# Kernel optimization log

Measured on AMD Instinct MI355X. Metric: run time of the kernel, lower is better.

The kernel has to match this reference:

```python
import jax, jax.numpy as jnp
import numpy as np
import math

B, S, L = 16, 512, 2400
TEXT_DIM, MAX_LEN, N_LAYERS = 64, 256, 6
LN_EPS = 1e-5


def conv1d(x, w, b, pad):
    # x: (B, Cin, W), w: (Cout, Cin, K) -> (B, Cout, W)
    y = jax.lax.conv_general_dilated(x, w, (1,), [(pad, pad)],
                                     dimension_numbers=('NCH', 'OIH', 'NCH'))
    if b is not None:
        y = y + b[None, :, None]
    return y


def setup_inputs() -> dict:
    key = jax.random.key(0)
    ks = jax.random.split(key, 16)
    inv_l = 1.0 / math.sqrt(L)
    inv_t = 1.0 / math.sqrt(TEXT_DIM)
    return {
        "slices": jax.random.normal(ks[0], (B, S, L), jnp.float32),
        "text_codes": jax.random.uniform(ks[1], (B, MAX_LEN), dtype=jnp.float32),
        # TextCondEncoder params
        "tc1_w": jax.random.normal(ks[2], (64, 1, 7), jnp.float32) * (1.0 / math.sqrt(7)),
        "tc1_b": jnp.zeros((64,), jnp.float32),
        "tc2_w": jax.random.normal(ks[3], (128, 64, 5), jnp.float32) * (1.0 / math.sqrt(64 * 5)),
        "tc2_b": jnp.zeros((128,), jnp.float32),
        "tc3_w": jax.random.normal(ks[4], (TEXT_DIM, 128, 3), jnp.float32) * (1.0 / math.sqrt(128 * 3)),
        "tc3_b": jnp.zeros((TEXT_DIM,), jnp.float32),
        # DecoderBlock params, stacked over layers
        "lin_w": jax.random.normal(ks[5], (N_LAYERS, L, L), jnp.float32) * inv_l,
        "lin_b": jnp.zeros((N_LAYERS, L), jnp.float32),
        "dconv_w": jax.random.normal(ks[6], (N_LAYERS, 1, 1, 9), jnp.float32) * (1.0 / 3.0),
        "bias_w": jax.random.normal(ks[7], (N_LAYERS, TEXT_DIM), jnp.float32) * inv_t,
        "bias_b": jnp.zeros((N_LAYERS,), jnp.float32),
        "gain_w": jax.random.normal(ks[8], (N_LAYERS, TEXT_DIM), jnp.float32) * inv_t,
        "gain_b": jnp.zeros((N_LAYERS,), jnp.float32),
        "ln_g": jnp.ones((N_LAYERS, L), jnp.float32),
        "ln_be": jnp.zeros((N_LAYERS, L), jnp.float32),
        "slices_mask": jnp.ones((B, S), dtype=bool),
        "total_steps": 32,
    }


def _text_encode(text_codes, tc1_w, tc1_b, tc2_w, tc2_b, tc3_w, tc3_b):
    # codepoints already normalized to [0,1]; torch GELU is exact (erf)
    x = text_codes[:, None, :]  # (B, 1, MAX_LEN)
    x = jax.nn.gelu(conv1d(x, tc1_w, tc1_b, 3), approximate=False)
    x = jax.nn.gelu(conv1d(x, tc2_w, tc2_b, 2), approximate=False)
    x = jax.nn.gelu(conv1d(x, tc3_w, tc3_b, 1), approximate=False)
    return jnp.mean(x, axis=-1)  # AdaptiveAvgPool1d(1) -> (B, TEXT_DIM)


def _generate(slices, slices_mask, text_cond, layer_params, total_steps):
    inv_sqrt_l = 1.0 / math.sqrt(L)
    neg_inf = jnp.asarray(-jnp.inf, slices.dtype)
    Bv = slices.shape[0]

    def layer_step(seg, lp):
        lw, lb, cw, bw, bb, gw, gb, g, be = lp
        # cross-correlation attention over raw slices
        dot = jnp.einsum('bl,bsl->bs', seg, slices) * inv_sqrt_l
        logits = dot + (text_cond @ bw + bb)[:, None]  # FiLM-like logit bias
        logits = jnp.where(slices_mask, logits, neg_inf)
        attn = jax.nn.softmax(logits, axis=-1)
        mixed = jnp.einsum('bs,bsl->bl', attn, slices)
        gain = jax.nn.sigmoid(text_cond @ gw + gb)[:, None]
        mixed = mixed * gain
        x = conv1d(mixed[:, None, :], cw, None, 4)[:, 0, :]  # smoothing conv k=9
        x = x + seg
        mu = jnp.mean(x, axis=-1, keepdims=True)
        var = jnp.var(x, axis=-1, keepdims=True)
        xn = (x - mu) * jax.lax.rsqrt(var + LN_EPS) * g + be  # LayerNorm(L)
        return xn @ lw.T + lb, None

    def step(seg, _):
        seg, _ = jax.lax.scan(layer_step, seg, layer_params)
        return seg, seg

    seg0 = jnp.zeros((Bv, L), slices.dtype)
    _, outs = jax.lax.scan(step, seg0, None, length=total_steps)  # (T, B, L)
    return jnp.transpose(outs, (1, 0, 2)).reshape(Bv, -1)  # cat over time -> (B, T*L)


def reference(slices, text_codes, tc1_w, tc1_b, tc2_w, tc2_b, tc3_w, tc3_b,
              lin_w, lin_b, dconv_w, bias_w, bias_b, gain_w, gain_b,
              ln_g, ln_be, slices_mask, total_steps):
    text_cond = _text_encode(text_codes, tc1_w, tc1_b, tc2_w, tc2_b, tc3_w, tc3_b)
    layer_params = (lin_w, lin_b, dconv_w, bias_w, bias_b, gain_w, gain_b, ln_g, ln_be)
    return _generate(slices, slices_mask, text_cond, layer_params, total_steps)
```

## Files before the change

### kernel.cpp

```cpp
#include <hip/hip_runtime.h>
#include <math.h>

#define B 16
#define S 512
#define L 2400
#define TD 64
#define ML 256
#define NL 6
#define STEPS 32
#define LN_EPS 1e-5f
#define INV_SQRT_L 0.020412414523193152f
#define G 32
#define RPW 4

__device__ __forceinline__ float gelu_exact(float x) {
    return 0.5f * x * (1.0f + erff(x * 0.7071067811865476f));
}

__global__ __launch_bounds__(256) void k_te1(const float* __restrict__ tc, const float* __restrict__ w,
                                             const float* __restrict__ bias, float* __restrict__ out1) {
    int idx = blockIdx.x * 256 + threadIdx.x;
    int p = idx & 255, oc = (idx >> 8) & 63, b = idx >> 14;
    const float* in = tc + b * ML;
    const float* wr = w + oc * 7;
    float acc = bias[oc];
#pragma unroll
    for (int k = 0; k < 7; ++k) {
        int q = p + k - 3;
        if (q >= 0 && q < ML) acc += in[q] * wr[k];
    }
    out1[idx] = gelu_exact(acc);
}

__global__ __launch_bounds__(256) void k_te2(const float* __restrict__ in1, const float* __restrict__ w,
                                             const float* __restrict__ bias, float* __restrict__ out2) {
    int idx = blockIdx.x * 256 + threadIdx.x;
    int p = idx & 255, oc = (idx >> 8) & 127, b = idx >> 15;
    const float* ib = in1 + b * 64 * ML;
    const float* wb = w + oc * 64 * 5;
    float acc = bias[oc];
    for (int ic = 0; ic < 64; ++ic) {
        const float* ir = ib + ic * ML;
        const float* wr = wb + ic * 5;
#pragma unroll
        for (int k = 0; k < 5; ++k) {
            int q = p + k - 2;
            if (q >= 0 && q < ML) acc += ir[q] * wr[k];
        }
    }
    out2[idx] = gelu_exact(acc);
}

__global__ __launch_bounds__(256) void k_te3(const float* __restrict__ in2, const float* __restrict__ w,
                                             const float* __restrict__ bias, float* __restrict__ tcond) {
    int b = blockIdx.x >> 6, oc = blockIdx.x & 63;
    int p = threadIdx.x;
    const float* ib = in2 + b * 128 * ML;
    const float* wb = w + oc * 128 * 3;
    float acc = bias[oc];
    for (int ic = 0; ic < 128; ++ic) {
        const float* ir = ib + ic * ML;
        const float* wr = wb + ic * 3;
        float s = ir[p] * wr[1];
        if (p > 0)      s += ir[p - 1] * wr[0];
        if (p < ML - 1) s += ir[p + 1] * wr[2];
        acc += s;
    }
    float v = gelu_exact(acc);
    __shared__ float red[4];
    for (int off = 32; off; off >>= 1) v += __shfl_xor(v, off);
    if ((threadIdx.x & 63) == 0) red[threadIdx.x >> 6] = v;
    __syncthreads();
    if (threadIdx.x == 0)
        tcond[b * TD + oc] = (red[0] + red[1] + red[2] + red[3]) * (1.0f / (float)ML);
}

__global__ __launch_bounds__(256) void k_uv(const float* __restrict__ lw, const float* __restrict__ g,
                                            const float* __restrict__ be,
                                            float* __restrict__ u, float* __restrict__ v) {
    int wv = threadIdx.x >> 6, lane = threadIdx.x & 63;
    int row = blockIdx.x * 4 + wv;
    int j = row / L;
    const float4* wr = (const float4*)(lw + (size_t)row * L);
    const float4* gr = (const float4*)(g + j * L);
    const float4* br = (const float4*)(be + j * L);
    float su = 0.f, sv = 0.f;
    for (int i = lane; i < L / 4; i += 64) {
        float4 w4 = wr[i], g4 = gr[i], b4 = br[i];
        su += w4.x * g4.x + w4.y * g4.y + w4.z * g4.z + w4.w * g4.w;
        sv += w4.x * b4.x + w4.y * b4.y + w4.z * b4.z + w4.w * b4.w;
    }
    for (int off = 32; off; off >>= 1) { su += __shfl_xor(su, off); sv += __shfl_xor(sv, off); }
    if (lane == 0) { u[row] = su; v[row] = sv; }
}

__global__ __launch_bounds__(256) void k_scalars(const float* __restrict__ tcond,
                                                 const float* __restrict__ bw, const float* __restrict__ bb,
                                                 const float* __restrict__ gw, const float* __restrict__ gb,
                                                 float* __restrict__ biasS, float* __restrict__ gainS,
                                                 float* __restrict__ seg0) {
    int t = blockIdx.x * 256 + threadIdx.x;
    if (t < NL * B) {
        int j = t >> 4, b = t & 15;
        float a = 0.f;
        for (int d = 0; d < TD; ++d) a += tcond[b * TD + d] * bw[j * TD + d];
        biasS[t] = a + bb[j];
    } else if (t < 2 * NL * B) {
        int u2 = t - NL * B;
        int j = u2 >> 4, b = u2 & 15;
        float a = 0.f;
        for (int d = 0; d < TD; ++d) a += tcond[b * TD + d] * gw[j * TD + d];
        gainS[u2] = 1.0f / (1.0f + expf(-(a + gb[j])));
    }
    for (int i = t; i < B * L; i += 64 * 256) seg0[i] = 0.0f;
}

__global__ __launch_bounds__(256) void k_attn(const float* __restrict__ slices,
                                              const float* __restrict__ seg,
                                              const int* __restrict__ mask,
                                              const float* __restrict__ biasS,
                                              float* __restrict__ part, float* __restrict__ hdr,
                                              float* __restrict__ stats) {
    __shared__ float4 cbuf[4][600];
    __shared__ float wred[8];
    int bid = blockIdx.x;
    int b = bid >> 5, grp = bid & 31;
    int wv = threadIdx.x >> 6, lane = threadIdx.x & 63;

    float4 segv[10];
    const float4* segp = (const float4*)(seg + b * L);
#pragma unroll
    for (int w = 0; w < 10; ++w) {
        int i = w * 64 + lane;
        segv[w] = (i < 600) ? segp[i] : make_float4(0.f, 0.f, 0.f, 0.f);
    }
    float4 accv[10];
#pragma unroll
    for (int w = 0; w < 10; ++w) accv[w] = make_float4(0.f, 0.f, 0.f, 0.f);

    float m = -INFINITY, z = 0.f;
    float bscale = biasS[b];
    int s0 = grp * (S / G) + wv * RPW;
    for (int r = 0; r < RPW; ++r) {
        int s = s0 + r;
        const float4* rp = (const float4*)(slices + ((size_t)b * S + s) * L);
        float4 rv[10];
#pragma unroll
        for (int w = 0; w < 10; ++w) {
            int i = w * 64 + lane;
            rv[w] = (i < 600) ? rp[i] : make_float4(0.f, 0.f, 0.f, 0.f);
        }
        float d = 0.f;
#pragma unroll
        for (int w = 0; w < 10; ++w)
            d += rv[w].x * segv[w].x + rv[w].y * segv[w].y + rv[w].z * segv[w].z + rv[w].w * segv[w].w;
#pragma unroll
        for (int off = 32; off; off >>= 1) d += __shfl_xor(d, off);
        if (mask[b * S + s]) {
            float logit = d * INV_SQRT_L + bscale;
            float p;
            if (logit > m) {
                float f = expf(m - logit);
                z *= f;
#pragma unroll
                for (int w = 0; w < 10; ++w) {
                    accv[w].x *= f; accv[w].y *= f; accv[w].z *= f; accv[w].w *= f;
                }
                m = logit; p = 1.0f;
            } else {
                p = expf(logit - m);
            }
            z += p;
#pragma unroll
            for (int w = 0; w < 10; ++w) {
                accv[w].x += p * rv[w].x; accv[w].y += p * rv[w].y;
                accv[w].z += p * rv[w].z; accv[w].w += p * rv[w].w;
            }
        }
    }

    if (lane == 0) wred[wv] = m;
    __syncthreads();
    float M = fmaxf(fmaxf(wred[0], wred[1]), fmaxf(wred[2], wred[3]));
    float f = (m == -INFINITY) ? 0.f : expf(m - M);
    if (lane == 0) wred[4 + wv] = z * f;
#pragma unroll
    for (int w = 0; w < 10; ++w) {
        int i = w * 64 + lane;
        if (i < 600) {
            float4 a = accv[w];
            a.x *= f; a.y *= f; a.z *= f; a.w *= f;
            cbuf[wv][i] = a;
        }
    }
    __syncthreads();
    float Z = wred[4] + wred[5] + wred[6] + wred[7];
    float4* pp = (float4*)part;
    for (int i = threadIdx.x; i < 600; i += 256) {
        float4 c0 = cbuf[0][i], c1 = cbuf[1][i], c2 = cbuf[2][i], c3 = cbuf[3][i];
        float4 o;
        o.x = c0.x + c1.x + c2.x + c3.x;
        o.y = c0.y + c1.y + c2.y + c3.y;
        o.z = c0.z + c1.z + c2.z + c3.z;
        o.w = c0.w + c1.w + c2.w + c3.w;
        pp[(size_t)bid * 600 + i] = o;
    }
    if (threadIdx.x == 0) { hdr[2 * bid] = M; hdr[2 * bid + 1] = Z; }
    if (bid == 0 && threadIdx.x < 2 * B) stats[threadIdx.x] = 0.f;
}

__global__ __launch_bounds__(256) void k_comb(const float* __restrict__ part, const float* __restrict__ hdr,
                                              const float* __restrict__ gainS, const float* __restrict__ cw,
                                              const float* __restrict__ seg,
                                              float* __restrict__ xbuf, float* __restrict__ stats) {
    __shared__ float sm[248];
    __shared__ float fld[G];
    __shared__ float red[9];
    int b = blockIdx.x / 10, ch = blockIdx.x % 10;
    int l0 = ch * 240;
    int t = threadIdx.x;

    if (t < 64) {
        float mg = (t < G) ? hdr[2 * (b * G + t)] : -INFINITY;
#pragma unroll
        for (int off = 32; off; off >>= 1) mg = fmaxf(mg, __shfl_xor(mg, off));
        if (t == 0) red[8] = mg;
    }
    __syncthreads();
    float M = red[8];
    if (t < 64) {
        float fg = 0.f, zg = 0.f;
        if (t < G) {
            float mg = hdr[2 * (b * G + t)];
            fg = (mg == -INFINITY) ? 0.f : expf(mg - M);
            zg = fg * hdr[2 * (b * G + t) + 1];
            fld[t] = fg;
        }
#pragma unroll
        for (int off = 32; off; off >>= 1) zg += __shfl_xor(zg, off);
        if (t == 0) red[0] = zg;
    }
    __syncthreads();
    float Z = red[0];
    float ginv = gainS[b] / Z;

    float v = 0.f;
    int c = l0 - 4 + t;
    if (t < 248) {
        if (c >= 0 && c < L) {
            for (int g2 = 0; g2 < G; ++g2)
                v += fld[g2] * part[((size_t)(b * G + g2)) * L + c];
            v *= ginv;
        }
        sm[t] = v;
    }
    __syncthreads();

    float s1 = 0.f, s2 = 0.f;
    if (t < 240) {
        float x = 0.f;
#pragma unroll
        for (int k = 0; k < 9; ++k) x += sm[t + k] * cw[k];
        x += seg[b * L + l0 + t];
        xbuf[b * L + l0 + t] = x;
        s1 = x; s2 = x * x;
    }
#pragma unroll
    for (int off = 32; off; off >>= 1) { s1 += __shfl_xor(s1, off); s2 += __shfl_xor(s2, off); }
    int wv = t >> 6;
    if ((t & 63) == 0) { red[wv] = s1; red[4 + wv] = s2; }
    __syncthreads();
    if (t == 0) {
        atomicAdd(&stats[2 * b], red[0] + red[1] + red[2] + red[3]);
        atomicAdd(&stats[2 * b + 1], red[4] + red[5] + red[6] + red[7]);
    }
}

__global__ __launch_bounds__(256) void k_lin(const float* __restrict__ xbuf, const float* __restrict__ stats,
                                             const float* __restrict__ g, const float* __restrict__ lw,
                                             const float* __restrict__ lb,
                                             const float* __restrict__ u, const float* __restrict__ v,
                                             float* __restrict__ segn, float* __restrict__ outp, int step) {
    __shared__ float4 sxg[B][64];
    __shared__ float smu[B], srr[B];
    int t = threadIdx.x;
    if (t < B) {
        float s1 = stats[2 * t], s2 = stats[2 * t + 1];
        float mu = s1 * (1.0f / (float)L);
        float var = s2 * (1.0f / (float)L) - mu * mu;
        smu[t] = mu;
        srr[t] = 1.0f / sqrtf(var + LN_EPS);
    }
    int rg = t >> 6, lane = t & 63;
    int lp = blockIdx.x * 4 + rg;
    float acc[B];
#pragma unroll
    for (int i = 0; i < B; ++i) acc[i] = 0.f;
    const float4* lwr = (const float4*)(lw + (size_t)lp * L);
    const float4* g4p = (const float4*)g;
    for (int tile = 0; tile < 10; ++tile) {
        int lt = tile * 256;
        __syncthreads();
        for (int i = t; i < B * 64; i += 256) {
            int bb = i >> 6, c4 = i & 63;
            float4 xv = make_float4(0.f, 0.f, 0.f, 0.f);
            if (lt + c4 * 4 < L) {
                int gi = (lt >> 2) + c4;
                xv = ((const float4*)(xbuf + bb * L))[gi];
                float4 gv = g4p[gi];
                xv.x *= gv.x; xv.y *= gv.y; xv.z *= gv.z; xv.w *= gv.w;
            }
            sxg[bb][c4] = xv;
        }
        __syncthreads();
        int colbase = lt + lane * 4;
        if (colbase < L) {
            float4 w4 = lwr[(lt >> 2) + lane];
#pragma unroll
            for (int bb = 0; bb < B; ++bb) {
                float4 xv = sxg[bb][lane];
                acc[bb] += xv.x * w4.x + xv.y * w4.y + xv.z * w4.z + xv.w * w4.w;
            }
        }
    }
#pragma unroll
    for (int off = 32; off; off >>= 1) {
#pragma unroll
        for (int bb = 0; bb < B; ++bb) acc[bb] += __shfl_xor(acc[bb], off);
    }
    if (lane == 0) {
        float ur = u[lp];
        float vr = v[lp] + lb[lp];
#pragma unroll
        for (int bb = 0; bb < B; ++bb) {
            float a = srr[bb] * (acc[bb] - smu[bb] * ur) + vr;
            segn[bb * L + lp] = a;
            if (outp) outp[bb * (STEPS * L) + step * L + lp] = a;
        }
    }
}

extern "C" void kernel_launch(void* const* d_in, const int* in_sizes, int n_in,
                              void* d_out, int out_size, void* d_ws, size_t ws_size,
                              hipStream_t stream) {
    const float* slices  = (const float*)d_in[0];
    const float* text    = (const float*)d_in[1];
    const float* tc1_w   = (const float*)d_in[2];
    const float* tc1_b   = (const float*)d_in[3];
    const float* tc2_w   = (const float*)d_in[4];
    const float* tc2_b   = (const float*)d_in[5];
    const float* tc3_w   = (const float*)d_in[6];
    const float* tc3_b   = (const float*)d_in[7];
    const float* lin_w   = (const float*)d_in[8];
    const float* lin_b   = (const float*)d_in[9];
    const float* dconv_w = (const float*)d_in[10];
    const float* bias_w  = (const float*)d_in[11];
    const float* bias_b  = (const float*)d_in[12];
    const float* gain_w  = (const float*)d_in[13];
    const float* gain_b  = (const float*)d_in[14];
    const float* ln_g    = (const float*)d_in[15];
    const float* ln_be   = (const float*)d_in[16];
    const int*   mask    = (const int*)d_in[17];
    float* out = (float*)d_out;

    float* W0    = (float*)d_ws;
    float* A     = W0 + 1024;
    float* tcond = W0;
    float* te1   = A;
    float* te2   = A + 262144;
    float* part  = A;
    float* hdr   = A + 1228800;
    float* biasS = A + 1229824;
    float* gainS = biasS + 96;
    float* xbuf  = gainS + 96;
    float* stats = xbuf + 38400;
    float* segA  = stats + 32;
    float* segB  = segA + 38400;
    float* U     = segB + 38400;
    float* V     = U + 14400;

    k_te1<<<1024, 256, 0, stream>>>(text, tc1_w, tc1_b, te1);
    k_te2<<<2048, 256, 0, stream>>>(te1, tc2_w, tc2_b, te2);
    k_te3<<<1024, 256, 0, stream>>>(te2, tc3_w, tc3_b, tcond);
    k_uv <<<3600, 256, 0, stream>>>(lin_w, ln_g, ln_be, U, V);
    k_scalars<<<64, 256, 0, stream>>>(tcond, bias_w, bias_b, gain_w, gain_b, biasS, gainS, segA);

    float* segc = segA;
    float* segn = segB;
    for (int step = 0; step < STEPS; ++step) {
        for (int j = 0; j < NL; ++j) {
            k_attn<<<B * G, 256, 0, stream>>>(slices, segc, mask, biasS + j * B, part, hdr, stats);
            k_comb<<<B * 10, 256, 0, stream>>>(part, hdr, gainS + j * B, dconv_w + j * 9,
                                               segc, xbuf, stats);
            k_lin<<<600, 256, 0, stream>>>(xbuf, stats, ln_g + j * L, lin_w + (size_t)j * L * L,
                                           lin_b + j * L, U + j * L, V + j * L, segn,
                                           (j == NL - 1) ? out : nullptr, step);
            float* tmp = segc; segc = segn; segn = tmp;
        }
    }
}
```

Measured before the change: 9.105 ms.

## Pair rows in attention, move LN gain to comb, double-buffer linear tiles

New measurement: 13.46 ms. 47.9% more time.

```diff
diff --git a/kernel.cpp b/kernel.cpp
--- a/kernel.cpp
+++ b/kernel.cpp
@@ -115,17 +115,17 @@
     for (int i = t; i < B * L; i += 64 * 256) seg0[i] = 0.0f;
 }
 
-__global__ __launch_bounds__(256) void k_attn(const float* __restrict__ slices,
-                                              const float* __restrict__ seg,
-                                              const int* __restrict__ mask,
-                                              const float* __restrict__ biasS,
-                                              float* __restrict__ part, float* __restrict__ hdr,
-                                              float* __restrict__ stats) {
+__global__ __launch_bounds__(256, 2) void k_attn(const float* __restrict__ slices,
+                                                 const float* __restrict__ seg,
+                                                 const int* __restrict__ mask,
+                                                 const float* __restrict__ biasS,
+                                                 float* __restrict__ part, float* __restrict__ hdr) {
     __shared__ float4 cbuf[4][600];
     __shared__ float wred[8];
     int bid = blockIdx.x;
     int b = bid >> 5, grp = bid & 31;
     int wv = threadIdx.x >> 6, lane = threadIdx.x & 63;
+    int t = threadIdx.x;
 
     float4 segv[10];
     const float4* segp = (const float4*)(seg + b * L);
@@ -141,41 +141,45 @@
     float m = -INFINITY, z = 0.f;
     float bscale = biasS[b];
     int s0 = grp * (S / G) + wv * RPW;
-    for (int r = 0; r < RPW; ++r) {
-        int s = s0 + r;
-        const float4* rp = (const float4*)(slices + ((size_t)b * S + s) * L);
-        float4 rv[10];
+#pragma unroll
+    for (int pr = 0; pr < RPW / 2; ++pr) {
+        int s = s0 + pr * 2;
+        const float4* rpa = (const float4*)(slices + ((size_t)b * S + s) * L);
+        const float4* rpb = rpa + 600;
+        float4 rva[10], rvb[10];
 #pragma unroll
         for (int w = 0; w < 10; ++w) {
             int i = w * 64 + lane;
-            rv[w] = (i < 600) ? rp[i] : make_float4(0.f, 0.f, 0.f, 0.f);
-        }
-        float d = 0.f;
-#pragma unroll
-        for (int w = 0; w < 10; ++w)
-            d += rv[w].x * segv[w].x + rv[w].y * segv[w].y + rv[w].z * segv[w].z + rv[w].w * segv[w].w;
-#pragma unroll
-        for (int off = 32; off; off >>= 1) d += __shfl_xor(d, off);
-        if (mask[b * S + s]) {
-            float logit = d * INV_SQRT_L + bscale;
-            float p;
-            if (logit > m) {
-                float f = expf(m - logit);
-                z *= f;
-#pragma unroll
-                for (int w = 0; w < 10; ++w) {
-                    accv[w].x *= f; accv[w].y *= f; accv[w].z *= f; accv[w].w *= f;
-                }
-                m = logit; p = 1.0f;
-            } else {
-                p = expf(logit - m);
+            if (i < 600) { rva[w] = rpa[i]; rvb[w] = rpb[i]; }
+            else { rva[w] = make_float4(0.f,0.f,0.f,0.f); rvb[w] = make_float4(0.f,0.f,0.f,0.f); }
+        }
+        float da = 0.f, db = 0.f;
+#pragma unroll
+        for (int w = 0; w < 10; ++w) {
+            da += rva[w].x * segv[w].x + rva[w].y * segv[w].y + rva[w].z * segv[w].z + rva[w].w * segv[w].w;
+            db += rvb[w].x * segv[w].x + rvb[w].y * segv[w].y + rvb[w].z * segv[w].z + rvb[w].w * segv[w].w;
+        }
+#pragma unroll
+        for (int off = 32; off; off >>= 1) {
+            da += __shfl_xor(da, off);
+            db += __shfl_xor(db, off);
+        }
+        float la = mask[b * S + s]     ? da * INV_SQRT_L + bscale : -INFINITY;
+        float lb = mask[b * S + s + 1] ? db * INV_SQRT_L + bscale : -INFINITY;
+        float mn = fmaxf(m, fmaxf(la, lb));
+        if (mn > -INFINITY) {
+            float f  = expf(m - mn);
+            float pa = expf(la - mn);
+            float pb = expf(lb - mn);
+            z = z * f + pa + pb;
+#pragma unroll
+            for (int w = 0; w < 10; ++w) {
+                accv[w].x = accv[w].x * f + pa * rva[w].x + pb * rvb[w].x;
+                accv[w].y = accv[w].y * f + pa * rva[w].y + pb * rvb[w].y;
+                accv[w].z = accv[w].z * f + pa * rva[w].z + pb * rvb[w].z;
+                accv[w].w = accv[w].w * f + pa * rva[w].w + pb * rvb[w].w;
             }
-            z += p;
-#pragma unroll
-            for (int w = 0; w < 10; ++w) {
-                accv[w].x += p * rv[w].x; accv[w].y += p * rv[w].y;
-                accv[w].z += p * rv[w].z; accv[w].w += p * rv[w].w;
-            }
+            m = mn;
         }
     }
 
@@ -196,7 +200,7 @@
     __syncthreads();
     float Z = wred[4] + wred[5] + wred[6] + wred[7];
     float4* pp = (float4*)part;
-    for (int i = threadIdx.x; i < 600; i += 256) {
+    for (int i = t; i < 600; i += 256) {
         float4 c0 = cbuf[0][i], c1 = cbuf[1][i], c2 = cbuf[2][i], c3 = cbuf[3][i];
         float4 o;
         o.x = c0.x + c1.x + c2.x + c3.x;
@@ -205,14 +209,14 @@
         o.w = c0.w + c1.w + c2.w + c3.w;
         pp[(size_t)bid * 600 + i] = o;
     }
-    if (threadIdx.x == 0) { hdr[2 * bid] = M; hdr[2 * bid + 1] = Z; }
-    if (bid == 0 && threadIdx.x < 2 * B) stats[threadIdx.x] = 0.f;
+    if (t == 0) { hdr[2 * bid] = M; hdr[2 * bid + 1] = Z; }
 }
 
 __global__ __launch_bounds__(256) void k_comb(const float* __restrict__ part, const float* __restrict__ hdr,
                                               const float* __restrict__ gainS, const float* __restrict__ cw,
+                                              const float* __restrict__ lng,
                                               const float* __restrict__ seg,
-                                              float* __restrict__ xbuf, float* __restrict__ stats) {
+                                              float* __restrict__ xg, float* __restrict__ statsP) {
     __shared__ float sm[248];
     __shared__ float fld[G];
     __shared__ float red[9];
@@ -262,7 +266,7 @@
 #pragma unroll
         for (int k = 0; k < 9; ++k) x += sm[t + k] * cw[k];
         x += seg[b * L + l0 + t];
-        xbuf[b * L + l0 + t] = x;
+        xg[b * L + l0 + t] = x * lng[l0 + t];
         s1 = x; s2 = x * x;
     }
 #pragma unroll
@@ -271,21 +275,25 @@
     if ((t & 63) == 0) { red[wv] = s1; red[4 + wv] = s2; }
     __syncthreads();
     if (t == 0) {
-        atomicAdd(&stats[2 * b], red[0] + red[1] + red[2] + red[3]);
-        atomicAdd(&stats[2 * b + 1], red[4] + red[5] + red[6] + red[7]);
-    }
-}
-
-__global__ __launch_bounds__(256) void k_lin(const float* __restrict__ xbuf, const float* __restrict__ stats,
-                                             const float* __restrict__ g, const float* __restrict__ lw,
-                                             const float* __restrict__ lb,
+        statsP[blockIdx.x * 2]     = red[0] + red[1] + red[2] + red[3];
+        statsP[blockIdx.x * 2 + 1] = red[4] + red[5] + red[6] + red[7];
+    }
+}
+
+__global__ __launch_bounds__(256) void k_lin(const float* __restrict__ xg, const float* __restrict__ statsP,
+                                             const float* __restrict__ lw, const float* __restrict__ lb,
                                              const float* __restrict__ u, const float* __restrict__ v,
                                              float* __restrict__ segn, float* __restrict__ outp, int step) {
-    __shared__ float4 sxg[B][64];
+    __shared__ float4 sxg[2][B][64];
     __shared__ float smu[B], srr[B];
     int t = threadIdx.x;
     if (t < B) {
-        float s1 = stats[2 * t], s2 = stats[2 * t + 1];
+        float s1 = 0.f, s2 = 0.f;
+#pragma unroll
+        for (int k = 0; k < 10; ++k) {
+            s1 += statsP[(t * 10 + k) * 2];
+            s2 += statsP[(t * 10 + k) * 2 + 1];
+        }
         float mu = s1 * (1.0f / (float)L);
         float var = s2 * (1.0f / (float)L) - mu * mu;
         smu[t] = mu;
@@ -297,31 +305,47 @@
 #pragma unroll
     for (int i = 0; i < B; ++i) acc[i] = 0.f;
     const float4* lwr = (const float4*)(lw + (size_t)lp * L);
-    const float4* g4p = (const float4*)g;
+    const float4* xg4 = (const float4*)xg;
+
+    float4 pf[4];
+#pragma unroll
+    for (int q = 0; q < 4; ++q) {
+        int i = t + q * 256;
+        pf[q] = xg4[(i >> 6) * 600 + (i & 63)];
+    }
+#pragma unroll
+    for (int q = 0; q < 4; ++q) {
+        int i = t + q * 256;
+        sxg[0][i >> 6][i & 63] = pf[q];
+    }
+    __syncthreads();
+
     for (int tile = 0; tile < 10; ++tile) {
-        int lt = tile * 256;
-        __syncthreads();
-        for (int i = t; i < B * 64; i += 256) {
-            int bb = i >> 6, c4 = i & 63;
-            float4 xv = make_float4(0.f, 0.f, 0.f, 0.f);
-            if (lt + c4 * 4 < L) {
-                int gi = (lt >> 2) + c4;
-                xv = ((const float4*)(xbuf + bb * L))[gi];
-                float4 gv = g4p[gi];
-                xv.x *= gv.x; xv.y *= gv.y; xv.z *= gv.z; xv.w *= gv.w;
+        if (tile < 9) {
+#pragma unroll
+            for (int q = 0; q < 4; ++q) {
+                int i = t + q * 256;
+                int gi = (tile + 1) * 64 + (i & 63);
+                pf[q] = (gi < 600) ? xg4[(i >> 6) * 600 + gi] : make_float4(0.f, 0.f, 0.f, 0.f);
             }
-            sxg[bb][c4] = xv;
-        }
-        __syncthreads();
-        int colbase = lt + lane * 4;
+        }
+        int colbase = tile * 256 + lane * 4;
         if (colbase < L) {
-            float4 w4 = lwr[(lt >> 2) + lane];
+            float4 w4 = lwr[tile * 64 + lane];
 #pragma unroll
             for (int bb = 0; bb < B; ++bb) {
-                float4 xv = sxg[bb][lane];
+                float4 xv = sxg[tile & 1][bb][lane];
                 acc[bb] += xv.x * w4.x + xv.y * w4.y + xv.z * w4.z + xv.w * w4.w;
             }
         }
+        if (tile < 9) {
+#pragma unroll
+            for (int q = 0; q < 4; ++q) {
+                int i = t + q * 256;
+                sxg[(tile + 1) & 1][i >> 6][i & 63] = pf[q];
+            }
+        }
+        __syncthreads();
     }
 #pragma unroll
     for (int off = 32; off; off >>= 1) {
@@ -364,17 +388,17 @@
     float* out = (float*)d_out;
 
     float* W0    = (float*)d_ws;
+    float* tcond = W0;
     float* A     = W0 + 1024;
-    float* tcond = W0;
     float* te1   = A;
     float* te2   = A + 262144;
     float* part  = A;
     float* hdr   = A + 1228800;
-    float* biasS = A + 1229824;
+    float* biasS = hdr + 1024;
     float* gainS = biasS + 96;
-    float* xbuf  = gainS + 96;
-    float* stats = xbuf + 38400;
-    float* segA  = stats + 32;
+    float* xg    = gainS + 96;
+    float* statsP= xg + 38400;
+    float* segA  = statsP + 320;
     float* segB  = segA + 38400;
     float* U     = segB + 38400;
     float* V     = U + 14400;
@@ -389,10 +413,10 @@
     float* segn = segB;
     for (int step = 0; step < STEPS; ++step) {
         for (int j = 0; j < NL; ++j) {
-            k_attn<<<B * G, 256, 0, stream>>>(slices, segc, mask, biasS + j * B, part, hdr, stats);
+            k_attn<<<B * G, 256, 0, stream>>>(slices, segc, mask, biasS + j * B, part, hdr);
             k_comb<<<B * 10, 256, 0, stream>>>(part, hdr, gainS + j * B, dconv_w + j * 9,
-                                               segc, xbuf, stats);
-            k_lin<<<600, 256, 0, stream>>>(xbuf, stats, ln_g + j * L, lin_w + (size_t)j * L * L,
+                                               ln_g + j * L, segc, xg, statsP);
+            k_lin<<<600, 256, 0, stream>>>(xg, statsP, lin_w + (size_t)j * L * L,
                                            lin_b + j * L, U + j * L, V + j * L, segn,
                                            (j == NL - 1) ? out : nullptr, step);
             float* tmp = segc; segc = segn; segn = tmp;
```
